# Performance work log

Hardware: AMD Instinct MI355X
Metric: run time of the kernel (lower is better)

The kernel has to match this reference:

```python
import jax, jax.numpy as jnp
import numpy as np

# ---- static skeleton topology (20 edges, humanoid: spine + 2 arms + 2 legs) ----
EDGES = [(0,1),(1,2),(2,3),(3,4),(3,5),(5,6),(6,7),(7,8),(3,9),(9,10),(10,11),(11,12),
         (0,13),(13,14),(14,15),(15,16),(0,17),(17,18),(18,19),(19,20)]
SKELETON_DIST = 2
IN_PER_J, OUT_PER_J = 64, 128
KSIZE, PAD, STRIDE = 15, 7, 2
BATCH, T = 8, 4096


def _calc_edge_mat(edges):
    n = len(edges)
    INF = 100000
    m = np.full((n, n), INF, dtype=np.int64)
    np.fill_diagonal(m, 0)
    for i, a in enumerate(edges):
        for j, b in enumerate(edges):
            if a[0] in b or a[1] in b:
                m[i, j] = min(m[i, j], 1)
    for k in range(n):  # Floyd-Warshall on tiny static graph
        m = np.minimum(m, m[:, k:k+1] + m[k:k+1, :])
    return m


def _find_neighbor(edges, d):
    m = _calc_edge_mat(edges)
    n = len(edges)
    neigh = [[j for j in range(n) if m[i, j] <= d] for i in range(n)]
    global_part = list(neigh[0])
    for i in global_part:
        neigh[i].append(n)  # virtual global edge index n
    neigh.append(global_part)
    return neigh


def _build_mask(neigh, in_pj, out_pj, k):
    J = len(neigh)
    mask = np.zeros((J * out_pj, J * in_pj, k), dtype=np.float32)
    for i, nb in enumerate(neigh):
        for j in nb:
            mask[i*out_pj:(i+1)*out_pj, j*in_pj:(j+1)*in_pj, :] = 1.0
    return mask


def _build_pool_weight(edges, cpe):
    degree = [0] * 100
    for e in edges:
        degree[e[0]] += 1
        degree[e[1]] += 1
    seq_list = []
    def find_seq(j, seq):
        if degree[j] > 2 and j != 0:
            seq_list.append(seq); seq = []
        if degree[j] == 1:
            seq_list.append(seq); return
        for idx, e in enumerate(edges):
            if e[0] == j:
                find_seq(e[1], seq + [idx])
    find_seq(0, [])
    pooling = []
    for seq in seq_list:
        seq = list(seq)
        if len(seq) % 2 == 1:
            pooling.append([seq[0]]); seq = seq[1:]
        for i in range(0, len(seq), 2):
            pooling.append([seq[i], seq[i+1]])
    edge_num = len(edges) + 1
    pooling.append([edge_num - 1])
    W = np.zeros((len(pooling) * cpe, edge_num * cpe), dtype=np.float32)
    for i, pair in enumerate(pooling):
        for j in pair:
            for c in range(cpe):
                W[i*cpe + c, j*cpe + c] = 1.0 / len(pair)
    return W


def setup_inputs() -> dict:
    key = jax.random.key(0)
    k1, k2, k3 = jax.random.split(key, 3)
    J = len(EDGES) + 1  # 21 (edges + virtual global)
    in_c, out_c = J * IN_PER_J, J * OUT_PER_J  # 1344, 2688
    neigh = _find_neighbor(EDGES, SKELETON_DIST)
    mask = jnp.asarray(_build_mask(neigh, IN_PER_J, OUT_PER_J, KSIZE))
    pool_w = jnp.asarray(_build_pool_weight(EDGES, out_c // J))
    x = jax.random.normal(k1, (BATCH, in_c, T), dtype=jnp.float32)
    weight = jax.random.normal(k2, (out_c, in_c, KSIZE), dtype=jnp.float32) * 0.02
    bias = jax.random.normal(k3, (out_c,), dtype=jnp.float32) * 0.01
    return {"x": x, "weight": weight, "bias": bias, "mask": mask, "pool_w": pool_w}


def reference(x, weight, bias, mask, pool_w):
    # SkeletonConv: per-joint neighbor mask applied to dense conv1d weights
    w = weight * mask  # [out_c, in_c, K]
    xp = jnp.pad(x, ((0, 0), (0, 0), (PAD, PAD)), mode='reflect')
    y = jax.lax.conv_general_dilated(
        xp, w, window_strides=(STRIDE,), padding='VALID',
        dimension_numbers=('NCH', 'OIH', 'NCH'))
    y = y + bias[None, :, None]  # [B, out_c, T//2]
    # SkeletonPool: mean over graph-defined edge groups via matmul
    p = jnp.einsum('pc,bct->bpt', pool_w, y)
    # LeakyReLU activation as in the layer stack
    return jax.nn.leaky_relu(p, negative_slope=0.2)
```

## Files before the change

### kernel.cpp

```cpp
#include <hip/hip_runtime.h>
#include <cstdint>
#include <cstddef>

typedef unsigned short u16;
typedef unsigned int   u32;

typedef __bf16 bf16x8 __attribute__((ext_vector_type(8)));
typedef float  f32x4  __attribute__((ext_vector_type(4)));

__constant__ int d_slot_jb[85] = {
  0,1,2,12,13,16,17,20,
  0,1,2,3,4,5,8,9,12,16,20,
  1,2,3,4,5,8,9,
  1,2,3,4,5,6,7,8,9,
  4,5,6,7,
  1,2,3,4,5,8,9,10,11,
  8,9,10,11,
  0,1,12,13,14,15,16,17,20,
  12,13,14,15,
  0,1,12,13,16,17,18,19,20,
  16,17,18,19,
  0,1,2,12,13,16,17
};
__constant__ int   d_gs0[12]    = {0,8,19,26,35,39,48,52,61,65,74,78};
__constant__ int   d_gnb[12]    = {8,11,7,9,4,9,4,9,4,9,4,7};
__constant__ int   d_gj0[12]    = {0,1,3,4,6,8,10,12,14,16,18,20};
__constant__ int   d_gj1[12]    = {-1,2,-1,5,7,9,11,13,15,17,19,-1};
__constant__ float d_gscale[12] = {1.f,0.5f,1.f,0.5f,0.5f,0.5f,0.5f,0.5f,0.5f,0.5f,0.5f,1.f};
__constant__ int   d_sched[12]  = {1,3,5,7,9,0,2,11,4,6,8,10};

static __device__ __forceinline__ u16 f2bf(float f) {
  union { float f; u32 u; } v; v.f = f;
  u32 r = v.u + 0x7fffu + ((v.u >> 16) & 1u);
  return (u16)(r >> 16);
}

__global__ void prep_x(const float* __restrict__ x, u16* __restrict__ xp) {
  int gid = blockIdx.x * 256 + threadIdx.x;
  if (gid >= 8 * 1344 * 514) return;
  int pc  = gid % 514;
  int row = gid / 514;
  int p   = pc * 8;
  const float* xr = x + (size_t)row * 4096;
  u16 v[8];
#pragma unroll
  for (int e = 0; e < 8; ++e) {
    int j = p + e - 7;
    j = j < 0 ? -j : (j > 4095 ? 8190 - j : j);
    v[e] = f2bf(xr[j]);
  }
  *(uint4*)(xp + (size_t)row * 4112 + p) = *(const uint4*)v;
}

__global__ void prep_w(const float* __restrict__ wt, const float* __restrict__ msk,
                       u16* __restrict__ apk) {
  int gid = blockIdx.x * 256 + threadIdx.x;
  if (gid >= 85 * 8192) return;
  int u   = gid >> 13;
  int rem = gid & 8191;
  int m   = rem >> 6;
  int c   = rem & 63;
  int g = 11;
#pragma unroll
  for (int gg = 0; gg < 11; ++gg)
    if (u >= d_gs0[gg] && u < d_gs0[gg + 1]) g = gg;
  int jb = d_slot_jb[u];
  int j0 = d_gj0[g], j1 = d_gj1[g];
  float sc = d_gscale[g];
  float m0 = msk[((size_t)(j0 * 128) * 1344 + jb * 64) * 15];
  float m1 = (j1 >= 0) ? msk[((size_t)(j1 * 128) * 1344 + jb * 64) * 15] : 0.f;
  const float* w0 = wt + ((size_t)(j0 * 128 + m) * 1344 + jb * 64 + c) * 15;
  const float* w1 = (j1 >= 0) ? wt + ((size_t)(j1 * 128 + m) * 1344 + jb * 64 + c) * 15 : w0;
  u16 v[16];
#pragma unroll
  for (int k = 0; k < 15; ++k) {
    float a = m0 * w0[k] + m1 * w1[k];
    v[k] = f2bf(a * sc);
  }
  v[15] = 0;
  uint4* dst = (uint4*)(apk + (size_t)u * 131072 + (c >> 1) * 4096 + m * 32 + (c & 1) * 16);
  dst[0] = ((const uint4*)v)[0];
  dst[1] = ((const uint4*)v)[1];
}

__global__ void prep_b(const float* __restrict__ bias, float* __restrict__ bg) {
  int pc = blockIdx.x * 256 + threadIdx.x;
  if (pc >= 1536) return;
  int g = pc >> 7, m = pc & 127;
  float v = bias[d_gj0[g] * 128 + m];
  if (d_gj1[g] >= 0) v += bias[d_gj1[g] * 128 + m];
  bg[pc] = v * d_gscale[g];
}

static __device__ __forceinline__ void load_a(bf16x8 dst[4], const u16* __restrict__ p) {
#pragma unroll
  for (int mt = 0; mt < 4; ++mt)
    dst[mt] = *(const bf16x8*)(p + mt * 512);
}

static __device__ __forceinline__ void compute_chunk(
    const bf16x8 af[4], const u32* __restrict__ xr32, int c32, f32x4 acc[4][4]) {
#pragma unroll
  for (int nt = 0; nt < 4; ++nt) {
    union { u32 u[4]; bf16x8 v; } bb;
#pragma unroll
    for (int ww = 0; ww < 4; ++ww)
      bb.u[ww] = xr32[c32 * 280 + nt * 16 + ww];
#pragma unroll
    for (int mt = 0; mt < 4; ++mt)
      acc[mt][nt] = __builtin_amdgcn_mfma_f32_16x16x32_bf16(af[mt], bb.v, acc[mt][nt], 0, 0, 0);
  }
}

__global__ __launch_bounds__(256, 3)
void conv_main(const u16* __restrict__ xpbf, const u16* __restrict__ apk,
               const float* __restrict__ biasg, float* __restrict__ out) {
  __shared__ __align__(16) u16 xs[64 * 280];

  const int tid = threadIdx.x;
  const int l   = tid & 63, w = tid >> 6;
  const int q   = l >> 4, lm = l & 15;
  const int wm  = w & 1, wn = w >> 1;

  const int gidx = blockIdx.x >> 7;
  const int g    = d_sched[gidx];
  const int r    = blockIdx.x & 127;
  const int b    = r >> 4;
  const int tile = r & 15;
  const int t0   = tile << 7;
  const int p0   = t0 << 1;

  const int nb = d_gnb[g];
  const int s0 = d_gs0[g];

  f32x4 acc[4][4];
#pragma unroll
  for (int i = 0; i < 4; ++i)
#pragma unroll
    for (int j = 0; j < 4; ++j)
      acc[i][j] = (f32x4){0.f, 0.f, 0.f, 0.f};

  const int a_off = (wm * 64 + lm) * 32 + q * 8;
  const u32* xr32 = (const u32*)(xs + (q >> 1) * 280 + (q & 1) * 8 + (wn * 64 + lm) * 2);

  bf16x8 afA[4], afB[4];

  for (int s = 0; s < nb; ++s) {
    const int u  = s0 + s;
    const int jb = d_slot_jb[u];
    __syncthreads();
    {
      const u16* srow = xpbf + (size_t)(b * 1344 + jb * 64) * 4112 + p0;
      for (int i = tid; i < 64 * 34; i += 256) {
        int c  = i / 34;
        int sg = i - c * 34;
        uint4 v = *(const uint4*)(srow + (size_t)c * 4112 + sg * 8);
        *(uint4*)((char*)xs + c * 560 + sg * 16) = v;
      }
    }
    __syncthreads();

    const u16* ap = apk + (size_t)u * 131072 + a_off;
    load_a(afA, ap);
#pragma unroll
    for (int k2 = 0; k2 < 16; ++k2) {
      load_a(afB, ap + 4096);
      compute_chunk(afA, xr32, 2 * k2, acc);
      if (k2 < 15) load_a(afA, ap + 8192);
      compute_chunk(afB, xr32, 2 * k2 + 1, acc);
      ap += 8192;
    }
  }

  const float* bgp = biasg + g * 128 + wm * 64;
  float* outb = out + ((size_t)b * 1536 + g * 128 + wm * 64) * 2048 + t0 + wn * 64;
#pragma unroll
  for (int mt = 0; mt < 4; ++mt) {
    const f32x4 bv = *(const f32x4*)(bgp + mt * 16 + q * 4);
#pragma unroll
    for (int reg = 0; reg < 4; ++reg) {
      const float bias = bv[reg];
      const int m = mt * 16 + q * 4 + reg;
      float* orow = outb + (size_t)m * 2048 + lm;
#pragma unroll
      for (int nt = 0; nt < 4; ++nt) {
        float v = acc[mt][nt][reg] + bias;
        orow[nt * 16] = v < 0.f ? 0.2f * v : v;
      }
    }
  }
}

extern "C" void kernel_launch(void* const* d_in, const int* in_sizes, int n_in,
                              void* d_out, int out_size, void* d_ws, size_t ws_size,
                              hipStream_t stream) {
  (void)in_sizes; (void)n_in; (void)out_size; (void)ws_size;
  const float* x   = (const float*)d_in[0];
  const float* wt  = (const float*)d_in[1];
  const float* bs  = (const float*)d_in[2];
  const float* msk = (const float*)d_in[3];

  u16*   xpbf = (u16*)d_ws;
  u16*   apk  = (u16*)((char*)d_ws + 88424448);
  float* bg   = (float*)((char*)d_ws + 110706688);
  float* out  = (float*)d_out;

  prep_x<<<dim3(21588), dim3(256), 0, stream>>>(x, xpbf);
  prep_w<<<dim3(2720),  dim3(256), 0, stream>>>(wt, msk, apk);
  prep_b<<<dim3(6),     dim3(256), 0, stream>>>(bs, bg);
  conv_main<<<dim3(1536), dim3(256), 0, stream>>>(xpbf, apk, bg, out);
}
```

Before: 874.1 us.

## Stage weight tiles into LDS via async global_load_lds double buffer; fuse prep kernels

Instead of each wave reading its A (weight) fragments straight from global memory into registers, the main conv kernel now stages each 4096-element weight chunk into a double-buffered, XOR-swizzled LDS area with global_load_lds. Each chunk is followed by barriers and a vmcnt wait. This is meant to share weight loads across the block and overlap them with MFMA work. It also adds two block-wide barriers per chunk (64 per slot) and extra LDS use, which may lower occupancy. The three prep kernels are merged into one launch to cut launch overhead.

```diff
diff --git a/kernel.cpp b/kernel.cpp
--- a/kernel.cpp
+++ b/kernel.cpp
@@ -7,6 +7,9 @@
 
 typedef __bf16 bf16x8 __attribute__((ext_vector_type(8)));
 typedef float  f32x4  __attribute__((ext_vector_type(4)));
+
+#define AS1C(p) ((const __attribute__((address_space(1))) void*)(p))
+#define AS3(p)  ((__attribute__((address_space(3))) void*)(p))
 
 __constant__ int d_slot_jb[85] = {
   0,1,2,12,13,16,17,20,
@@ -35,71 +38,84 @@
   return (u16)(r >> 16);
 }
 
-__global__ void prep_x(const float* __restrict__ x, u16* __restrict__ xp) {
-  int gid = blockIdx.x * 256 + threadIdx.x;
-  if (gid >= 8 * 1344 * 514) return;
-  int pc  = gid % 514;
-  int row = gid / 514;
-  int p   = pc * 8;
-  const float* xr = x + (size_t)row * 4096;
-  u16 v[8];
-#pragma unroll
-  for (int e = 0; e < 8; ++e) {
-    int j = p + e - 7;
-    j = j < 0 ? -j : (j > 4095 ? 8190 - j : j);
-    v[e] = f2bf(xr[j]);
-  }
-  *(uint4*)(xp + (size_t)row * 4112 + p) = *(const uint4*)v;
-}
-
-__global__ void prep_w(const float* __restrict__ wt, const float* __restrict__ msk,
-                       u16* __restrict__ apk) {
-  int gid = blockIdx.x * 256 + threadIdx.x;
-  if (gid >= 85 * 8192) return;
-  int u   = gid >> 13;
-  int rem = gid & 8191;
-  int m   = rem >> 6;
-  int c   = rem & 63;
-  int g = 11;
-#pragma unroll
-  for (int gg = 0; gg < 11; ++gg)
-    if (u >= d_gs0[gg] && u < d_gs0[gg + 1]) g = gg;
-  int jb = d_slot_jb[u];
-  int j0 = d_gj0[g], j1 = d_gj1[g];
-  float sc = d_gscale[g];
-  float m0 = msk[((size_t)(j0 * 128) * 1344 + jb * 64) * 15];
-  float m1 = (j1 >= 0) ? msk[((size_t)(j1 * 128) * 1344 + jb * 64) * 15] : 0.f;
-  const float* w0 = wt + ((size_t)(j0 * 128 + m) * 1344 + jb * 64 + c) * 15;
-  const float* w1 = (j1 >= 0) ? wt + ((size_t)(j1 * 128 + m) * 1344 + jb * 64 + c) * 15 : w0;
-  u16 v[16];
-#pragma unroll
-  for (int k = 0; k < 15; ++k) {
-    float a = m0 * w0[k] + m1 * w1[k];
-    v[k] = f2bf(a * sc);
-  }
-  v[15] = 0;
-  uint4* dst = (uint4*)(apk + (size_t)u * 131072 + (c >> 1) * 4096 + m * 32 + (c & 1) * 16);
-  dst[0] = ((const uint4*)v)[0];
-  dst[1] = ((const uint4*)v)[1];
-}
-
-__global__ void prep_b(const float* __restrict__ bias, float* __restrict__ bg) {
-  int pc = blockIdx.x * 256 + threadIdx.x;
-  if (pc >= 1536) return;
-  int g = pc >> 7, m = pc & 127;
-  float v = bias[d_gj0[g] * 128 + m];
-  if (d_gj1[g] >= 0) v += bias[d_gj1[g] * 128 + m];
-  bg[pc] = v * d_gscale[g];
-}
-
-static __device__ __forceinline__ void load_a(bf16x8 dst[4], const u16* __restrict__ p) {
+__global__ void prep_all(const float* __restrict__ x, const float* __restrict__ wt,
+                         const float* __restrict__ msk, const float* __restrict__ bias,
+                         u16* __restrict__ xp, u16* __restrict__ apk,
+                         float* __restrict__ bg) {
+  const int blk = blockIdx.x;
+  if (blk < 2720) {
+    int gid = blk * 256 + threadIdx.x;
+    if (gid >= 85 * 8192) return;
+    int u   = gid >> 13;
+    int rem = gid & 8191;
+    int m   = rem >> 6;
+    int c   = rem & 63;
+    int g = 11;
+#pragma unroll
+    for (int gg = 0; gg < 11; ++gg)
+      if (u >= d_gs0[gg] && u < d_gs0[gg + 1]) g = gg;
+    int jb = d_slot_jb[u];
+    int j0 = d_gj0[g], j1 = d_gj1[g];
+    float sc = d_gscale[g];
+    float m0 = msk[((size_t)(j0 * 128) * 1344 + jb * 64) * 15];
+    float m1 = (j1 >= 0) ? msk[((size_t)(j1 * 128) * 1344 + jb * 64) * 15] : 0.f;
+    const float* w0 = wt + ((size_t)(j0 * 128 + m) * 1344 + jb * 64 + c) * 15;
+    const float* w1 = (j1 >= 0) ? wt + ((size_t)(j1 * 128 + m) * 1344 + jb * 64 + c) * 15 : w0;
+    u16 v[16];
+#pragma unroll
+    for (int k = 0; k < 15; ++k) {
+      float a = m0 * w0[k] + m1 * w1[k];
+      v[k] = f2bf(a * sc);
+    }
+    v[15] = 0;
+    uint4* dst = (uint4*)(apk + (size_t)u * 131072 + (c >> 1) * 4096 + m * 32 + (c & 1) * 16);
+    dst[0] = ((const uint4*)v)[0];
+    dst[1] = ((const uint4*)v)[1];
+  } else if (blk < 24308) {
+    int gid = (blk - 2720) * 256 + threadIdx.x;
+    if (gid >= 8 * 1344 * 514) return;
+    int pc  = gid % 514;
+    int row = gid / 514;
+    int p   = pc * 8;
+    const float* xr = x + (size_t)row * 4096;
+    u16 v[8];
+#pragma unroll
+    for (int e = 0; e < 8; ++e) {
+      int j = p + e - 7;
+      j = j < 0 ? -j : (j > 4095 ? 8190 - j : j);
+      v[e] = f2bf(xr[j]);
+    }
+    *(uint4*)(xp + (size_t)row * 4112 + p) = *(const uint4*)v;
+  } else {
+    int pc = (blk - 24308) * 256 + threadIdx.x;
+    if (pc >= 1536) return;
+    int g = pc >> 7, m = pc & 127;
+    float v = bias[d_gj0[g] * 128 + m];
+    if (d_gj1[g] >= 0) v += bias[d_gj1[g] * 128 + m];
+    bg[pc] = v * d_gscale[g];
+  }
+}
+
+static __device__ __forceinline__ void stage_a(const u16* __restrict__ src,
+                                               char* dst, int tid) {
+  const int w = tid >> 6;
+#pragma unroll
+  for (int ii = 0; ii < 2; ++ii) {
+    const int seg = ii * 256 + tid;
+    const int m   = seg >> 2;
+    const int s   = (seg & 3) ^ ((m >> 1) & 3);
+    __builtin_amdgcn_global_load_lds(AS1C(src + m * 32 + s * 8),
+                                     AS3(dst + ii * 4096 + w * 1024), 16, 0, 0);
+  }
+}
+
+static __device__ __forceinline__ void compute_chunk_lds(
+    const char* __restrict__ abase, const u32* __restrict__ xr32, int c32,
+    f32x4 acc[4][4]) {
+  bf16x8 af[4];
 #pragma unroll
   for (int mt = 0; mt < 4; ++mt)
-    dst[mt] = *(const bf16x8*)(p + mt * 512);
-}
-
-static __device__ __forceinline__ void compute_chunk(
-    const bf16x8 af[4], const u32* __restrict__ xr32, int c32, f32x4 acc[4][4]) {
+    af[mt] = *(const bf16x8*)(abase + mt * 1024);
 #pragma unroll
   for (int nt = 0; nt < 4; ++nt) {
     union { u32 u[4]; bf16x8 v; } bb;
@@ -116,6 +132,7 @@
 void conv_main(const u16* __restrict__ xpbf, const u16* __restrict__ apk,
                const float* __restrict__ biasg, float* __restrict__ out) {
   __shared__ __align__(16) u16 xs[64 * 280];
+  __shared__ __align__(16) u16 as[2 * 4096];
 
   const int tid = threadIdx.x;
   const int l   = tid & 63, w = tid >> 6;
@@ -140,14 +157,16 @@
     for (int j = 0; j < 4; ++j)
       acc[i][j] = (f32x4){0.f, 0.f, 0.f, 0.f};
 
-  const int a_off = (wm * 64 + lm) * 32 + q * 8;
+  const char* a0 = (const char*)as + (wm * 64 + lm) * 64 + ((q ^ ((lm >> 1) & 3)) << 4);
+  const char* a1 = a0 + 8192;
   const u32* xr32 = (const u32*)(xs + (q >> 1) * 280 + (q & 1) * 8 + (wn * 64 + lm) * 2);
 
-  bf16x8 afA[4], afB[4];
+  const u16* ablk = apk + (size_t)s0 * 131072;
+  stage_a(ablk, (char*)as, tid);
+  stage_a(ablk + 4096, (char*)as + 8192, tid);
 
   for (int s = 0; s < nb; ++s) {
-    const int u  = s0 + s;
-    const int jb = d_slot_jb[u];
+    const int jb = d_slot_jb[s0 + s];
     __syncthreads();
     {
       const u16* srow = xpbf + (size_t)(b * 1344 + jb * 64) * 4112 + p0;
@@ -160,17 +179,23 @@
     }
     __syncthreads();
 
-    const u16* ap = apk + (size_t)u * 131072 + a_off;
-    load_a(afA, ap);
-#pragma unroll
-    for (int k2 = 0; k2 < 16; ++k2) {
-      load_a(afB, ap + 4096);
-      compute_chunk(afA, xr32, 2 * k2, acc);
-      if (k2 < 15) load_a(afA, ap + 8192);
-      compute_chunk(afB, xr32, 2 * k2 + 1, acc);
-      ap += 8192;
-    }
-  }
+    const u16* nxt = (s + 1 < nb) ? ablk + 131072 : ablk;
+#pragma unroll
+    for (int c = 0; c < 32; ++c) {
+      compute_chunk_lds((c & 1) ? a1 : a0, xr32, c, acc);
+      __builtin_amdgcn_sched_barrier(0);
+      __builtin_amdgcn_s_barrier();
+      __builtin_amdgcn_sched_barrier(0);
+      const u16* src = (c < 30) ? (ablk + (c + 2) * 4096) : (nxt + (c - 30) * 4096);
+      stage_a(src, (char*)as + (c & 1) * 8192, tid);
+      asm volatile("s_waitcnt vmcnt(2)" ::: "memory");
+      __builtin_amdgcn_sched_barrier(0);
+      __builtin_amdgcn_s_barrier();
+      __builtin_amdgcn_sched_barrier(0);
+    }
+    ablk = nxt;
+  }
+  asm volatile("s_waitcnt vmcnt(0)" ::: "memory");
 
   const float* bgp = biasg + g * 128 + wm * 64;
   float* outb = out + ((size_t)b * 1536 + g * 128 + wm * 64) * 2048 + t0 + wn * 64;
@@ -205,8 +230,6 @@
   float* bg   = (float*)((char*)d_ws + 110706688);
   float* out  = (float*)d_out;
 
-  prep_x<<<dim3(21588), dim3(256), 0, stream>>>(x, xpbf);
-  prep_w<<<dim3(2720),  dim3(256), 0, stream>>>(wt, msk, apk);
-  prep_b<<<dim3(6),     dim3(256), 0, stream>>>(bs, bg);
+  prep_all<<<dim3(24314), dim3(256), 0, stream>>>(x, wt, msk, bs, xpbf, apk, bg);
   conv_main<<<dim3(1536), dim3(256), 0, stream>>>(xpbf, apk, bg, out);
 }
```

After: 983.4 us. +12.5%, slower.
